# Optimization experiments

Measured on AMD Instinct MI355X. Metric: run time of the kernel, lower is better.

Reference implementation:

```python
import jax, jax.numpy as jnp
import numpy as np

DIM = 768
NUM_HEADS = 12
HEAD_DIM = DIM // NUM_HEADS
PATCH_H = 64
PATCH_W = 64
SCALE = HEAD_DIM ** -0.5


def setup_inputs() -> dict:
    key = jax.random.key(0)
    k1, k2, k3, k4 = jax.random.split(key, 4)
    x = jax.random.normal(k1, (16, PATCH_H * PATCH_W, DIM), dtype=jnp.float32)
    # torch Linear stores weight as (out, in); y = x @ W.T. Keep same convention.
    w_qkv = jax.random.normal(k2, (3 * DIM, DIM), dtype=jnp.float32) * (DIM ** -0.5)
    w_proj = jax.random.normal(k3, (DIM, DIM), dtype=jnp.float32) * (DIM ** -0.5)
    b_proj = jax.random.normal(k4, (DIM,), dtype=jnp.float32) * 0.01
    return {"x": x, "w_qkv": w_qkv, "w_proj": w_proj, "b_proj": b_proj}


def reference(x, w_qkv, w_proj, b_proj):
    B, N, C = x.shape
    H, W = PATCH_H, PATCH_W
    nh, hd = NUM_HEADS, HEAD_DIM
    # group rows: each row of W tokens attends only within itself
    xg = x.reshape(B * H, W, C)                      # (G, W, C)
    qkv = xg @ w_qkv.T                                # (G, W, 3C)
    qkv = qkv.reshape(B * H, W, 3, nh, hd)
    q = qkv[:, :, 0].transpose(0, 2, 1, 3)           # (G, nh, W, hd)
    k = qkv[:, :, 1].transpose(0, 2, 1, 3)
    v = qkv[:, :, 2].transpose(0, 2, 1, 3)
    attn = jnp.einsum('ghqd,ghkd->ghqk', q, k) * SCALE
    attn = jax.nn.softmax(attn, axis=-1)
    out = jnp.einsum('ghqk,ghkd->ghqd', attn, v)      # (G, nh, W, hd)
    out = out.transpose(0, 2, 1, 3).reshape(B * H, W, C)
    out = out @ w_proj.T + b_proj
    return out.reshape(B, N, C)
```

## Files before the change

### kernel.cpp

```cpp
#include <hip/hip_runtime.h>


#define SCALE 0.125f

typedef _Float16 h16;
typedef h16   half8 __attribute__((ext_vector_type(8)));
typedef float f32x4 __attribute__((ext_vector_type(4)));

typedef const __attribute__((address_space(1))) unsigned int ga_u32;
typedef __attribute__((address_space(3))) unsigned int ls_u32;

__device__ __forceinline__ void cvt8(const float* __restrict__ s,
                                     h16* __restrict__ d, int i) {
  const float4 a = ((const float4*)s)[2 * i];
  const float4 b = ((const float4*)s)[2 * i + 1];
  half8 r;
  r[0] = (h16)a.x; r[1] = (h16)a.y; r[2] = (h16)a.z; r[3] = (h16)a.w;
  r[4] = (h16)b.x; r[5] = (h16)b.y; r[6] = (h16)b.z; r[7] = (h16)b.w;
  ((half8*)d)[i] = r;
}

__global__ void prep_cvt(const float* __restrict__ wq, const float* __restrict__ wp,
                         const float* __restrict__ x,
                         h16* __restrict__ wq16, h16* __restrict__ wp16,
                         h16* __restrict__ xh) {
  const int stride = gridDim.x * blockDim.x;
  const int t0 = blockIdx.x * blockDim.x + threadIdx.x;
  for (int i = t0; i < 221184; i += stride) cvt8(wq, wq16, i);
  for (int i = t0; i < 73728;  i += stride) cvt8(wp, wp16, i);
  for (int i = t0; i < 6291456; i += stride) cvt8(x, xh, i);
}

__global__ void prep_w_only(const float* __restrict__ wq, const float* __restrict__ wp,
                            h16* __restrict__ wq16, h16* __restrict__ wp16) {
  const int stride = gridDim.x * blockDim.x;
  const int t0 = blockIdx.x * blockDim.x + threadIdx.x;
  for (int i = t0; i < 221184; i += stride) cvt8(wq, wq16, i);
  for (int i = t0; i < 73728;  i += stride) cvt8(wp, wp16, i);
}

__global__ __launch_bounds__(256)
void qkv_attn(const h16* __restrict__ A,
              const h16* __restrict__ B,
              h16* __restrict__ O) {
  __shared__ h16 smem[40960];
  h16* As0 = smem;
  h16* Bs0 = smem + 16384;
  h16* sQ  = smem;
  h16* sK  = smem + 9216;
  h16* sV  = smem + 18432;

  const int nwg = gridDim.x;
  const int bid = blockIdx.x;
  const int wg  = (bid & 7) * (nwg >> 3) + (bid >> 3);
  const int mt = wg / 12, h = wg - mt * 12;
  const int m0 = mt * 128;

  const int tid  = threadIdx.x;
  const int lane = tid & 63;
  const int wv   = tid >> 6;
  const int l16  = lane & 15;
  const int kg   = lane >> 4;
  const int wr   = wv >> 1;
  const int wc   = wv & 1;

  const int srow = tid >> 3;
  const int cg   = (tid & 7) ^ (srow & 7);
  const h16* pA[4];
  const h16* pB[6];
  int loA[4], loB[6];
  #pragma unroll
  for (int i = 0; i < 4; ++i) {
    const int r = i * 32 + srow;
    pA[i]  = A + (size_t)(m0 + r) * 768 + cg * 8;
    loA[i] = (i * 256 + tid) * 8;
  }
  #pragma unroll
  for (int i = 0; i < 6; ++i) {
    const int r  = i * 32 + srow;
    const int gr = (r >> 6) * 768 + h * 64 + (r & 63);
    pB[i]  = B + (size_t)gr * 768 + cg * 8;
    loB[i] = (i * 256 + tid) * 8;
  }

#define GLDS(srcp, ldsp)                                                       \
  __builtin_amdgcn_global_load_lds((ga_u32*)(const void*)(srcp),               \
                                   (ls_u32*)(void*)(ldsp), 16, 0, 0)
#define STAGE(bf, kt)                                                          \
  do {                                                                         \
    GLDS(pA[0] + (kt) * 64, &As0[(bf) * 8192 + loA[0]]);                       \
    GLDS(pA[1] + (kt) * 64, &As0[(bf) * 8192 + loA[1]]);                       \
    GLDS(pA[2] + (kt) * 64, &As0[(bf) * 8192 + loA[2]]);                       \
    GLDS(pA[3] + (kt) * 64, &As0[(bf) * 8192 + loA[3]]);                       \
    GLDS(pB[0] + (kt) * 64, &Bs0[(bf) * 12288 + loB[0]]);                      \
    GLDS(pB[1] + (kt) * 64, &Bs0[(bf) * 12288 + loB[1]]);                      \
    GLDS(pB[2] + (kt) * 64, &Bs0[(bf) * 12288 + loB[2]]);                      \
    GLDS(pB[3] + (kt) * 64, &Bs0[(bf) * 12288 + loB[3]]);                      \
    GLDS(pB[4] + (kt) * 64, &Bs0[(bf) * 12288 + loB[4]]);                      \
    GLDS(pB[5] + (kt) * 64, &Bs0[(bf) * 12288 + loB[5]]);                      \
  } while (0)

  const int aBase = (wr * 64 + l16) * 64;
  const int bBase = (wc * 96 + l16) * 64;
  int axor[2];
  #pragma unroll
  for (int ks = 0; ks < 2; ++ks)
    axor[ks] = ((ks * 4 + kg) ^ (l16 & 7)) * 8;

  f32x4 acc[4][6];
  #pragma unroll
  for (int mi = 0; mi < 4; ++mi)
    #pragma unroll
    for (int ni = 0; ni < 6; ++ni)
      acc[mi][ni] = (f32x4){0.f, 0.f, 0.f, 0.f};

  STAGE(0, 0);
  asm volatile("s_waitcnt vmcnt(0)" ::: "memory");
  __syncthreads();

  int cur = 0;
  for (int t = 0; t < 12; ++t) {
    if (t < 11) STAGE(cur ^ 1, t + 1);
    const h16* Ac = As0 + cur * 8192;
    const h16* Bc = Bs0 + cur * 12288;
    #pragma unroll
    for (int ks = 0; ks < 2; ++ks) {
      half8 af[4], bf8[6];
      #pragma unroll
      for (int mi = 0; mi < 4; ++mi)
        af[mi] = *(const half8*)&Ac[aBase + mi * 1024 + axor[ks]];
      #pragma unroll
      for (int ni = 0; ni < 6; ++ni)
        bf8[ni] = *(const half8*)&Bc[bBase + ni * 1024 + axor[ks]];
      #pragma unroll
      for (int mi = 0; mi < 4; ++mi)
        #pragma unroll
        for (int ni = 0; ni < 6; ++ni)
          acc[mi][ni] = __builtin_amdgcn_mfma_f32_16x16x32_f16(af[mi], bf8[ni], acc[mi][ni], 0, 0, 0);
    }
    asm volatile("s_waitcnt vmcnt(0)" ::: "memory");
    __syncthreads();
    cur ^= 1;
  }
#undef STAGE
#undef GLDS

  #pragma unroll
  for (int mi = 0; mi < 4; ++mi) {
    const int rowb = wr * 64 + mi * 16 + kg * 4;
    const int r6   = (rowb & 63);
    #pragma unroll
    for (int ni = 0; ni < 6; ++ni) {
      const int cbase = wc * 96 + ni * 16;
      const int sel = cbase >> 6;
      const int d   = (cbase & 63) + l16;
      if (sel == 0) {
        #pragma unroll
        for (int j = 0; j < 4; ++j) sQ[(rowb + j) * 72 + d] = (h16)acc[mi][ni][j];
      } else if (sel == 1) {
        #pragma unroll
        for (int j = 0; j < 4; ++j) sK[(rowb + j) * 72 + d] = (h16)acc[mi][ni][j];
      } else {
        #pragma unroll
        for (int j = 0; j < 4; ++j) sV[wr * 4608 + d * 72 + r6 + j] = (h16)acc[mi][ni][j];
      }
    }
  }
  __syncthreads();

  const int qr0 = wr * 64 + wc * 32;

  f32x4 sacc[2][4];
  #pragma unroll
  for (int rb = 0; rb < 2; ++rb)
    #pragma unroll
    for (int cb = 0; cb < 4; ++cb) sacc[rb][cb] = (f32x4){0.f, 0.f, 0.f, 0.f};

  #pragma unroll
  for (int ks = 0; ks < 2; ++ks) {
    half8 aq[2];
    #pragma unroll
    for (int rb = 0; rb < 2; ++rb)
      aq[rb] = *(const half8*)&sQ[(qr0 + rb * 16 + l16) * 72 + ks * 32 + kg * 8];
    #pragma unroll
    for (int cb = 0; cb < 4; ++cb) {
      const half8 kf = *(const half8*)&sK[(wr * 64 + cb * 16 + l16) * 72 + ks * 32 + kg * 8];
      #pragma unroll
      for (int rb = 0; rb < 2; ++rb)
        sacc[rb][cb] = __builtin_amdgcn_mfma_f32_16x16x32_f16(aq[rb], kf, sacc[rb][cb], 0, 0, 0);
    }
  }

  float e[2][4][4];
  #pragma unroll
  for (int rb = 0; rb < 2; ++rb) {
    float rs[4];
    #pragma unroll
    for (int j = 0; j < 4; ++j) {
      float t = 0.f;
      #pragma unroll
      for (int cb = 0; cb < 4; ++cb) { e[rb][cb][j] = __expf(sacc[rb][cb][j] * SCALE); t += e[rb][cb][j]; }
      rs[j] = t;
    }
    #pragma unroll
    for (int m = 1; m < 16; m <<= 1)
      #pragma unroll
      for (int j = 0; j < 4; ++j) rs[j] += __shfl_xor(rs[j], m);
    #pragma unroll
    for (int j = 0; j < 4; ++j) rs[j] = __fdividef(1.0f, rs[j]);
    #pragma unroll
    for (int cb = 0; cb < 4; ++cb)
      #pragma unroll
      for (int j = 0; j < 4; ++j)
        sQ[(qr0 + rb * 16 + kg * 4 + j) * 72 + cb * 16 + l16] = (h16)(e[rb][cb][j] * rs[j]);
  }
  __syncthreads();

  f32x4 oacc[2][4];
  #pragma unroll
  for (int rb = 0; rb < 2; ++rb)
    #pragma unroll
    for (int cb = 0; cb < 4; ++cb) oacc[rb][cb] = (f32x4){0.f, 0.f, 0.f, 0.f};
  #pragma unroll
  for (int ks = 0; ks < 2; ++ks) {
    half8 ap[2];
    #pragma unroll
    for (int rb = 0; rb < 2; ++rb)
      ap[rb] = *(const half8*)&sQ[(qr0 + rb * 16 + l16) * 72 + ks * 32 + kg * 8];
    #pragma unroll
    for (int cb = 0; cb < 4; ++cb) {
      const half8 vf = *(const half8*)&sV[wr * 4608 + (cb * 16 + l16) * 72 + ks * 32 + kg * 8];
      #pragma unroll
      for (int rb = 0; rb < 2; ++rb)
        oacc[rb][cb] = __builtin_amdgcn_mfma_f32_16x16x32_f16(ap[rb], vf, oacc[rb][cb], 0, 0, 0);
    }
  }

  #pragma unroll
  for (int rb = 0; rb < 2; ++rb)
    #pragma unroll
    for (int cb = 0; cb < 4; ++cb)
      #pragma unroll
      for (int j = 0; j < 4; ++j)
        sK[(qr0 + rb * 16 + kg * 4 + j) * 72 + cb * 16 + l16] = (h16)oacc[rb][cb][j];
  __syncthreads();
  #pragma unroll
  for (int c = tid; c < 1024; c += 256) {
    const int row = c >> 3, d0 = (c & 7) * 8;
    *(half8*)(O + (size_t)(m0 + row) * 768 + h * 64 + d0) = *(const half8*)&sK[row * 72 + d0];
  }
}

template <bool BIAS, typename OutT>
__global__ void gemm_bt(const h16* __restrict__ A, int lda,
                        const h16* __restrict__ B,
                        const float* __restrict__ bias,
                        OutT* __restrict__ C, int ldc,
                        int ntiles) {
  __shared__ h16 As[2][4096];
  __shared__ h16 Bs[2][4096];

  const int nwg = gridDim.x;
  const int bid = blockIdx.x;
  const int wg  = (bid & 7) * (nwg >> 3) + (bid >> 3);
  const int mt = wg / ntiles, nt = wg - mt * ntiles;
  const int m0 = mt * 128, n0 = nt * 128;

  const int tid  = threadIdx.x;
  const int lane = tid & 63;
  const int wv   = tid >> 6;
  const int l16  = lane & 15;
  const int kg   = lane >> 4;

  const h16* pa[2];
  const h16* pb[2];
  int lo[2];
  #pragma unroll
  for (int i = 0; i < 2; ++i) {
    const int row = wv * 32 + i * 16 + (lane >> 2);
    const int cg  = (lane & 3) ^ ((row >> 1) & 3);
    pa[i] = A + (size_t)(m0 + row) * lda + cg * 8;
    pb[i] = B + (size_t)(n0 + row) * 768 + cg * 8;
    lo[i] = wv * 1024 + i * 512;
  }

#define STAGE(bf, koff)                                                        \
  do {                                                                         \
    __builtin_amdgcn_global_load_lds((ga_u32*)(const void*)(pa[0] + (koff)),   \
                                     (ls_u32*)(void*)&As[bf][lo[0]], 16, 0, 0);\
    __builtin_amdgcn_global_load_lds((ga_u32*)(const void*)(pb[0] + (koff)),   \
                                     (ls_u32*)(void*)&Bs[bf][lo[0]], 16, 0, 0);\
    __builtin_amdgcn_global_load_lds((ga_u32*)(const void*)(pa[1] + (koff)),   \
                                     (ls_u32*)(void*)&As[bf][lo[1]], 16, 0, 0);\
    __builtin_amdgcn_global_load_lds((ga_u32*)(const void*)(pb[1] + (koff)),   \
                                     (ls_u32*)(void*)&Bs[bf][lo[1]], 16, 0, 0);\
  } while (0)

  const int s   = (l16 >> 1) & 3;
  const int wr  = wv >> 1, wc = wv & 1;
  const int ofA = (wr * 64 + l16) * 32 + ((kg ^ s) * 8);
  const int ofB = (wc * 64 + l16) * 32 + ((kg ^ s) * 8);

  f32x4 acc[4][4];
  #pragma unroll
  for (int mi = 0; mi < 4; ++mi)
    #pragma unroll
    for (int ni = 0; ni < 4; ++ni)
      acc[mi][ni] = (f32x4){0.f, 0.f, 0.f, 0.f};

  STAGE(0, 0);
  asm volatile("s_waitcnt vmcnt(0)" ::: "memory");
  __syncthreads();

  int cur = 0;
  for (int t = 0; t < 24; ++t) {
    if (t < 23) STAGE(cur ^ 1, (t + 1) * 32);
    half8 af[4], bf8[4];
    #pragma unroll
    for (int mi = 0; mi < 4; ++mi) af[mi]  = *(const half8*)&As[cur][ofA + mi * 512];
    #pragma unroll
    for (int ni = 0; ni < 4; ++ni) bf8[ni] = *(const half8*)&Bs[cur][ofB + ni * 512];
    #pragma unroll
    for (int mi = 0; mi < 4; ++mi)
      #pragma unroll
      for (int ni = 0; ni < 4; ++ni)
        acc[mi][ni] = __builtin_amdgcn_mfma_f32_16x16x32_f16(af[mi], bf8[ni], acc[mi][ni], 0, 0, 0);
    asm volatile("s_waitcnt vmcnt(0)" ::: "memory");
    __syncthreads();
    cur ^= 1;
  }
#undef STAGE

  float bv[4];
  if (BIAS) {
    #pragma unroll
    for (int ni = 0; ni < 4; ++ni) bv[ni] = bias[n0 + wc * 64 + ni * 16 + l16];
  }
  #pragma unroll
  for (int mi = 0; mi < 4; ++mi) {
    #pragma unroll
    for (int ni = 0; ni < 4; ++ni) {
      const int col = n0 + wc * 64 + ni * 16 + l16;
      #pragma unroll
      for (int j = 0; j < 4; ++j) {
        const int row = m0 + wr * 64 + mi * 16 + kg * 4 + j;
        if (BIAS) C[(size_t)row * ldc + col] = (OutT)(acc[mi][ni][j] + bv[ni]);
        else      C[(size_t)row * ldc + col] = (OutT)acc[mi][ni][j];
      }
    }
  }
}

template <typename WT>
__device__ __forceinline__ half8 loadw8(const WT* p);
template <>
__device__ __forceinline__ half8 loadw8<h16>(const h16* p) { return *(const half8*)p; }
template <>
__device__ __forceinline__ half8 loadw8<float>(const float* p) {
  const float4 a = *(const float4*)p;
  const float4 b = *(const float4*)(p + 4);
  half8 r;
  r[0] = (h16)a.x; r[1] = (h16)a.y; r[2] = (h16)a.z; r[3] = (h16)a.w;
  r[4] = (h16)b.x; r[5] = (h16)b.y; r[6] = (h16)b.z; r[7] = (h16)b.w;
  return r;
}

template <typename WT>
__launch_bounds__(512, 2)
__global__ void fused_fb(const float* __restrict__ x,
                         const WT* __restrict__ wq,
                         const WT* __restrict__ wp,
                         const float* __restrict__ bias,
                         float* __restrict__ out) {
  __shared__ h16   xs[64][776];
  __shared__ h16   qs[64][72];
  __shared__ h16   ks[64][72];
  __shared__ h16   vt[64][72];
  __shared__ float sS[64][68];

  const int g = blockIdx.x, tid = threadIdx.x;
  const int wv = tid >> 6, lane = tid & 63, l16 = lane & 15, kg = lane >> 4;

  const float* xg = x + (size_t)g * (64 * 768);
  #pragma unroll
  for (int i = 0; i < 24; ++i) {
    const int idx = tid + i * 512;
    const int row = idx / 192;
    const int c4  = (idx - row * 192) * 4;
    const float4 v = ((const float4*)xg)[idx];
    h16* p = &xs[row][c4];
    p[0] = (h16)v.x; p[1] = (h16)v.y; p[2] = (h16)v.z; p[3] = (h16)v.w;
  }

  f32x4 acc[4][6];
  #pragma unroll
  for (int a = 0; a < 4; ++a)
    #pragma unroll
    for (int b = 0; b < 6; ++b) acc[a][b] = (f32x4){0.f, 0.f, 0.f, 0.f};

  float bcol[6];
  #pragma unroll
  for (int cb = 0; cb < 6; ++cb) bcol[cb] = bias[wv * 96 + cb * 16 + l16];

  const int r0 = (wv & 1) * 32, c0 = (wv >> 1) * 48;
  const int rS = (wv >> 1) * 16, cS = (wv & 1) * 32;
  __syncthreads();

  for (int h = 0; h < 12; ++h) {
    f32x4 facc[2][3];
    #pragma unroll
    for (int a = 0; a < 2; ++a)
      #pragma unroll
      for (int b = 0; b < 3; ++b) facc[a][b] = (f32x4){0.f, 0.f, 0.f, 0.f};
    int wrow[3];
    #pragma unroll
    for (int cb = 0; cb < 3; ++cb) {
      const int n = c0 + cb * 16;
      wrow[cb] = (n >> 6) * 768 + h * 64 + (n & 63) + l16;
    }
    for (int k0 = 0; k0 < 768; k0 += 32) {
      const half8 a0 = *(const half8*)&xs[r0 + l16][k0 + kg * 8];
      const half8 a1 = *(const half8*)&xs[r0 + 16 + l16][k0 + kg * 8];
      #pragma unroll
      for (int cb = 0; cb < 3; ++cb) {
        const half8 b = loadw8<WT>(wq + (size_t)wrow[cb] * 768 + k0 + kg * 8);
        facc[0][cb] = __builtin_amdgcn_mfma_f32_16x16x32_f16(a0, b, facc[0][cb], 0, 0, 0);
        facc[1][cb] = __builtin_amdgcn_mfma_f32_16x16x32_f16(a1, b, facc[1][cb], 0, 0, 0);
      }
    }
    #pragma unroll
    for (int rb = 0; rb < 2; ++rb)
      #pragma unroll
      for (int cb = 0; cb < 3; ++cb) {
        const int col = c0 + cb * 16 + l16;
        const int rowb = r0 + rb * 16 + kg * 4;
        if (col < 64) {
          #pragma unroll
          for (int j = 0; j < 4; ++j) qs[rowb + j][col] = (h16)facc[rb][cb][j];
        } else if (col < 128) {
          #pragma unroll
          for (int j = 0; j < 4; ++j) ks[rowb + j][col - 64] = (h16)facc[rb][cb][j];
        } else {
          #pragma unroll
          for (int j = 0; j < 4; ++j) vt[col - 128][rowb + j] = (h16)facc[rb][cb][j];
        }
      }
    __syncthreads();

    f32x4 sacc[2];
    sacc[0] = (f32x4){0.f, 0.f, 0.f, 0.f};
    sacc[1] = (f32x4){0.f, 0.f, 0.f, 0.f};
    #pragma unroll
    for (int k0 = 0; k0 < 64; k0 += 32) {
      const half8 aq = *(const half8*)&qs[rS + l16][k0 + kg * 8];
      const half8 b0 = *(const half8*)&ks[cS + l16][k0 + kg * 8];
      const half8 b1 = *(const half8*)&ks[cS + 16 + l16][k0 + kg * 8];
      sacc[0] = __builtin_amdgcn_mfma_f32_16x16x32_f16(aq, b0, sacc[0], 0, 0, 0);
      sacc[1] = __builtin_amdgcn_mfma_f32_16x16x32_f16(aq, b1, sacc[1], 0, 0, 0);
    }
    #pragma unroll
    for (int t = 0; t < 2; ++t)
      #pragma unroll
      for (int j = 0; j < 4; ++j)
        sS[rS + kg * 4 + j][cS + t * 16 + l16] = sacc[t][j] * SCALE;
    __syncthreads();

    {
      const int row = tid >> 3, j0 = (tid & 7) * 8;
      float v0[8];
      #pragma unroll
      for (int i = 0; i < 8; ++i) v0[i] = sS[row][j0 + i];
      float m = v0[0];
      #pragma unroll
      for (int i = 1; i < 8; ++i) m = fmaxf(m, v0[i]);
      m = fmaxf(m, __shfl_xor(m, 1));
      m = fmaxf(m, __shfl_xor(m, 2));
      m = fmaxf(m, __shfl_xor(m, 4));
      float e[8], ssum = 0.f;
      #pragma unroll
      for (int i = 0; i < 8; ++i) { e[i] = __expf(v0[i] - m); ssum += e[i]; }
      ssum += __shfl_xor(ssum, 1);
      ssum += __shfl_xor(ssum, 2);
      ssum += __shfl_xor(ssum, 4);
      const float inv = 1.0f / ssum;
      #pragma unroll
      for (int i = 0; i < 8; ++i) qs[row][j0 + i] = (h16)(e[i] * inv);
    }
    __syncthreads();

    f32x4 oacc[2];
    oacc[0] = (f32x4){0.f, 0.f, 0.f, 0.f};
    oacc[1] = (f32x4){0.f, 0.f, 0.f, 0.f};
    #pragma unroll
    for (int k0 = 0; k0 < 64; k0 += 32) {
      const half8 ap = *(const half8*)&qs[rS + l16][k0 + kg * 8];
      const half8 b0 = *(const half8*)&vt[cS + l16][k0 + kg * 8];
      const half8 b1 = *(const half8*)&vt[cS + 16 + l16][k0 + kg * 8];
      oacc[0] = __builtin_amdgcn_mfma_f32_16x16x32_f16(ap, b0, oacc[0], 0, 0, 0);
      oacc[1] = __builtin_amdgcn_mfma_f32_16x16x32_f16(ap, b1, oacc[1], 0, 0, 0);
    }
    #pragma unroll
    for (int t = 0; t < 2; ++t)
      #pragma unroll
      for (int j = 0; j < 4; ++j)
        ks[rS + kg * 4 + j][cS + t * 16 + l16] = (h16)oacc[t][j];
    __syncthreads();

    #pragma unroll
    for (int k0 = 0; k0 < 64; k0 += 32) {
      half8 ah[4];
      #pragma unroll
      for (int rb = 0; rb < 4; ++rb)
        ah[rb] = *(const half8*)&ks[rb * 16 + l16][k0 + kg * 8];
      #pragma unroll
      for (int cb = 0; cb < 6; ++cb) {
        const int ocol = wv * 96 + cb * 16 + l16;
        const half8 bw = loadw8<WT>(wp + (size_t)ocol * 768 + h * 64 + k0 + kg * 8);
        #pragma unroll
        for (int rb = 0; rb < 4; ++rb)
          acc[rb][cb] = __builtin_amdgcn_mfma_f32_16x16x32_f16(ah[rb], bw, acc[rb][cb], 0, 0, 0);
      }
    }
    __syncthreads();
  }

  float* og = out + (size_t)g * (64 * 768);
  #pragma unroll
  for (int rb = 0; rb < 4; ++rb)
    #pragma unroll
    for (int cb = 0; cb < 6; ++cb) {
      const int col = wv * 96 + cb * 16 + l16;
      #pragma unroll
      for (int j = 0; j < 4; ++j) {
        const int row = rb * 16 + kg * 4 + j;
        og[(size_t)row * 768 + col] = acc[rb][cb][j] + bcol[cb];
      }
    }
}

extern "C" void kernel_launch(void* const* d_in, const int* in_sizes, int n_in,
                              void* d_out, int out_size, void* d_ws, size_t ws_size,
                              hipStream_t stream) {
  const float* x     = (const float*)d_in[0];
  const float* wqkv  = (const float*)d_in[1];
  const float* wproj = (const float*)d_in[2];
  const float* bias  = (const float*)d_in[3];
  float* out = (float*)d_out;

  const size_t SZ_WQ = (size_t)2304 * 768 * sizeof(h16);
  const size_t SZ_WP = (size_t)768 * 768 * sizeof(h16);
  const size_t SZ_XH = (size_t)65536 * 768 * sizeof(h16);
  const size_t SZ_O  = (size_t)65536 * 768 * sizeof(h16);

  if (ws_size >= SZ_WQ + SZ_WP + SZ_XH + SZ_O) {
    h16* wq16 = (h16*)d_ws;
    h16* wp16 = (h16*)((char*)d_ws + SZ_WQ);
    h16* xh   = (h16*)((char*)d_ws + SZ_WQ + SZ_WP);
    h16* obuf = (h16*)((char*)d_ws + SZ_WQ + SZ_WP + SZ_XH);

    prep_cvt<<<2048, 256, 0, stream>>>(wqkv, wproj, x, wq16, wp16, xh);
    qkv_attn<<<6144, 256, 0, stream>>>(xh, wq16, obuf);
    gemm_bt<true, float><<<3072, 256, 0, stream>>>(obuf, 768, wp16, bias, out, 768, 6);
  } else if (ws_size >= SZ_WQ + SZ_WP) {
    h16* wq16 = (h16*)d_ws;
    h16* wp16 = (h16*)((char*)d_ws + SZ_WQ);
    prep_w_only<<<512, 256, 0, stream>>>(wqkv, wproj, wq16, wp16);
    fused_fb<h16><<<1024, 512, 0, stream>>>(x, wq16, wp16, bias, out);
  } else {
    fused_fb<float><<<1024, 512, 0, stream>>>(x, wqkv, wproj, bias, out);
  }
}
```

Baseline: 476.3 us.

## Use 512-thread blocks in fused QKV-attention kernel with XOR-swizzled LDS layout

Doubles the qkv_attn workgroup from 4 to 8 waves, so each wave computes a 32x96 QKV tile instead of 64x96 and handles 16 query rows in attention instead of 32. This halves the accumulator registers per wave, which can raise occupancy and hide latency. The padded stride-72 LDS layout for Q/K/V is replaced by an XOR-swizzled stride-64 layout, with a matching unswizzle on the final store. The cost is more waves contending for the same LDS tiles and extra barrier participants. Per-wave B-fragment reuse also drops.

```diff
diff --git a/kernel.cpp b/kernel.cpp
--- a/kernel.cpp
+++ b/kernel.cpp
@@ -9,6 +9,8 @@
 
 typedef const __attribute__((address_space(1))) unsigned int ga_u32;
 typedef __attribute__((address_space(3))) unsigned int ls_u32;
+
+#define SWZ(r, c) (((r) << 6) + ((((c) >> 3) ^ ((r) & 7)) << 3) + ((c) & 7))
 
 __device__ __forceinline__ void cvt8(const float* __restrict__ s,
                                      h16* __restrict__ d, int i) {
@@ -39,7 +41,7 @@
   for (int i = t0; i < 73728;  i += stride) cvt8(wp, wp16, i);
 }
 
-__global__ __launch_bounds__(256)
+__global__ __launch_bounds__(512, 4)
 void qkv_attn(const h16* __restrict__ A,
               const h16* __restrict__ B,
               h16* __restrict__ O) {
@@ -47,8 +49,8 @@
   h16* As0 = smem;
   h16* Bs0 = smem + 16384;
   h16* sQ  = smem;
-  h16* sK  = smem + 9216;
-  h16* sV  = smem + 18432;
+  h16* sK  = smem + 8192;
+  h16* sV  = smem + 16384;
 
   const int nwg = gridDim.x;
   const int bid = blockIdx.x;
@@ -61,26 +63,27 @@
   const int wv   = tid >> 6;
   const int l16  = lane & 15;
   const int kg   = lane >> 4;
-  const int wr   = wv >> 1;
-  const int wc   = wv & 1;
+  const int wr   = wv & 3;
+  const int wc   = wv >> 2;
 
   const int srow = tid >> 3;
-  const int cg   = (tid & 7) ^ (srow & 7);
-  const h16* pA[4];
-  const h16* pB[6];
-  int loA[4], loB[6];
-  #pragma unroll
-  for (int i = 0; i < 4; ++i) {
-    const int r = i * 32 + srow;
+  const int slot = tid & 7;
+  const int cg   = slot ^ (srow & 7);
+  const h16* pA[2];
+  const h16* pB[3];
+  int loA[2], loB[3];
+  #pragma unroll
+  for (int i = 0; i < 2; ++i) {
+    const int r = i * 64 + srow;
     pA[i]  = A + (size_t)(m0 + r) * 768 + cg * 8;
-    loA[i] = (i * 256 + tid) * 8;
-  }
-  #pragma unroll
-  for (int i = 0; i < 6; ++i) {
-    const int r  = i * 32 + srow;
+    loA[i] = r * 64 + slot * 8;
+  }
+  #pragma unroll
+  for (int i = 0; i < 3; ++i) {
+    const int r  = i * 64 + srow;
     const int gr = (r >> 6) * 768 + h * 64 + (r & 63);
     pB[i]  = B + (size_t)gr * 768 + cg * 8;
-    loB[i] = (i * 256 + tid) * 8;
+    loB[i] = r * 64 + slot * 8;
   }
 
 #define GLDS(srcp, ldsp)                                                       \
@@ -90,26 +93,21 @@
   do {                                                                         \
     GLDS(pA[0] + (kt) * 64, &As0[(bf) * 8192 + loA[0]]);                       \
     GLDS(pA[1] + (kt) * 64, &As0[(bf) * 8192 + loA[1]]);                       \
-    GLDS(pA[2] + (kt) * 64, &As0[(bf) * 8192 + loA[2]]);                       \
-    GLDS(pA[3] + (kt) * 64, &As0[(bf) * 8192 + loA[3]]);                       \
     GLDS(pB[0] + (kt) * 64, &Bs0[(bf) * 12288 + loB[0]]);                      \
     GLDS(pB[1] + (kt) * 64, &Bs0[(bf) * 12288 + loB[1]]);                      \
     GLDS(pB[2] + (kt) * 64, &Bs0[(bf) * 12288 + loB[2]]);                      \
-    GLDS(pB[3] + (kt) * 64, &Bs0[(bf) * 12288 + loB[3]]);                      \
-    GLDS(pB[4] + (kt) * 64, &Bs0[(bf) * 12288 + loB[4]]);                      \
-    GLDS(pB[5] + (kt) * 64, &Bs0[(bf) * 12288 + loB[5]]);                      \
   } while (0)
 
-  const int aBase = (wr * 64 + l16) * 64;
+  const int aBase = (wr * 32 + l16) * 64;
   const int bBase = (wc * 96 + l16) * 64;
   int axor[2];
   #pragma unroll
   for (int ks = 0; ks < 2; ++ks)
     axor[ks] = ((ks * 4 + kg) ^ (l16 & 7)) * 8;
 
-  f32x4 acc[4][6];
-  #pragma unroll
-  for (int mi = 0; mi < 4; ++mi)
+  f32x4 acc[2][6];
+  #pragma unroll
+  for (int mi = 0; mi < 2; ++mi)
     #pragma unroll
     for (int ni = 0; ni < 6; ++ni)
       acc[mi][ni] = (f32x4){0.f, 0.f, 0.f, 0.f};
@@ -125,15 +123,15 @@
     const h16* Bc = Bs0 + cur * 12288;
     #pragma unroll
     for (int ks = 0; ks < 2; ++ks) {
-      half8 af[4], bf8[6];
-      #pragma unroll
-      for (int mi = 0; mi < 4; ++mi)
+      half8 af[2], bf8[6];
+      #pragma unroll
+      for (int mi = 0; mi < 2; ++mi)
         af[mi] = *(const half8*)&Ac[aBase + mi * 1024 + axor[ks]];
       #pragma unroll
       for (int ni = 0; ni < 6; ++ni)
         bf8[ni] = *(const half8*)&Bc[bBase + ni * 1024 + axor[ks]];
       #pragma unroll
-      for (int mi = 0; mi < 4; ++mi)
+      for (int mi = 0; mi < 2; ++mi)
         #pragma unroll
         for (int ni = 0; ni < 6; ++ni)
           acc[mi][ni] = __builtin_amdgcn_mfma_f32_16x16x32_f16(af[mi], bf8[ni], acc[mi][ni], 0, 0, 0);
@@ -146,9 +144,10 @@
 #undef GLDS
 
   #pragma unroll
-  for (int mi = 0; mi < 4; ++mi) {
-    const int rowb = wr * 64 + mi * 16 + kg * 4;
-    const int r6   = (rowb & 63);
+  for (int mi = 0; mi < 2; ++mi) {
+    const int rowb = wr * 32 + mi * 16 + kg * 4;
+    const int r6   = rowb & 63;
+    const int g2s  = rowb >> 6;
     #pragma unroll
     for (int ni = 0; ni < 6; ++ni) {
       const int cbase = wc * 96 + ni * 16;
@@ -156,98 +155,83 @@
       const int d   = (cbase & 63) + l16;
       if (sel == 0) {
         #pragma unroll
-        for (int j = 0; j < 4; ++j) sQ[(rowb + j) * 72 + d] = (h16)acc[mi][ni][j];
+        for (int j = 0; j < 4; ++j) sQ[SWZ(rowb + j, d)] = (h16)acc[mi][ni][j];
       } else if (sel == 1) {
         #pragma unroll
-        for (int j = 0; j < 4; ++j) sK[(rowb + j) * 72 + d] = (h16)acc[mi][ni][j];
+        for (int j = 0; j < 4; ++j) sK[SWZ(rowb + j, d)] = (h16)acc[mi][ni][j];
       } else {
         #pragma unroll
-        for (int j = 0; j < 4; ++j) sV[wr * 4608 + d * 72 + r6 + j] = (h16)acc[mi][ni][j];
+        for (int j = 0; j < 4; ++j) sV[g2s * 4096 + SWZ(d, r6 + j)] = (h16)acc[mi][ni][j];
       }
     }
   }
   __syncthreads();
 
-  const int qr0 = wr * 64 + wc * 32;
-
-  f32x4 sacc[2][4];
-  #pragma unroll
-  for (int rb = 0; rb < 2; ++rb)
-    #pragma unroll
-    for (int cb = 0; cb < 4; ++cb) sacc[rb][cb] = (f32x4){0.f, 0.f, 0.f, 0.f};
-
+  const int qr0 = wv * 16;
+  const int g2  = wv >> 2;
+  const h16* sKg = sK + g2 * 4096;
+  const h16* sVg = sV + g2 * 4096;
+
+  f32x4 sacc[4];
+  #pragma unroll
+  for (int cb = 0; cb < 4; ++cb) sacc[cb] = (f32x4){0.f, 0.f, 0.f, 0.f};
   #pragma unroll
   for (int ks = 0; ks < 2; ++ks) {
-    half8 aq[2];
-    #pragma unroll
-    for (int rb = 0; rb < 2; ++rb)
-      aq[rb] = *(const half8*)&sQ[(qr0 + rb * 16 + l16) * 72 + ks * 32 + kg * 8];
+    const half8 aq = *(const half8*)&sQ[(qr0 + l16) * 64 + axor[ks]];
     #pragma unroll
     for (int cb = 0; cb < 4; ++cb) {
-      const half8 kf = *(const half8*)&sK[(wr * 64 + cb * 16 + l16) * 72 + ks * 32 + kg * 8];
-      #pragma unroll
-      for (int rb = 0; rb < 2; ++rb)
-        sacc[rb][cb] = __builtin_amdgcn_mfma_f32_16x16x32_f16(aq[rb], kf, sacc[rb][cb], 0, 0, 0);
-    }
-  }
-
-  float e[2][4][4];
-  #pragma unroll
-  for (int rb = 0; rb < 2; ++rb) {
-    float rs[4];
-    #pragma unroll
-    for (int j = 0; j < 4; ++j) {
-      float t = 0.f;
-      #pragma unroll
-      for (int cb = 0; cb < 4; ++cb) { e[rb][cb][j] = __expf(sacc[rb][cb][j] * SCALE); t += e[rb][cb][j]; }
-      rs[j] = t;
-    }
-    #pragma unroll
-    for (int m = 1; m < 16; m <<= 1)
-      #pragma unroll
-      for (int j = 0; j < 4; ++j) rs[j] += __shfl_xor(rs[j], m);
-    #pragma unroll
-    for (int j = 0; j < 4; ++j) rs[j] = __fdividef(1.0f, rs[j]);
-    #pragma unroll
-    for (int cb = 0; cb < 4; ++cb)
-      #pragma unroll
-      for (int j = 0; j < 4; ++j)
-        sQ[(qr0 + rb * 16 + kg * 4 + j) * 72 + cb * 16 + l16] = (h16)(e[rb][cb][j] * rs[j]);
-  }
+      const half8 kf = *(const half8*)&sKg[(cb * 16 + l16) * 64 + axor[ks]];
+      sacc[cb] = __builtin_amdgcn_mfma_f32_16x16x32_f16(aq, kf, sacc[cb], 0, 0, 0);
+    }
+  }
+
+  float e[4][4], rs[4];
+  #pragma unroll
+  for (int j = 0; j < 4; ++j) {
+    float t = 0.f;
+    #pragma unroll
+    for (int cb = 0; cb < 4; ++cb) { e[cb][j] = __expf(sacc[cb][j] * SCALE); t += e[cb][j]; }
+    rs[j] = t;
+  }
+  #pragma unroll
+  for (int m = 1; m < 16; m <<= 1)
+    #pragma unroll
+    for (int j = 0; j < 4; ++j) rs[j] += __shfl_xor(rs[j], m);
+  #pragma unroll
+  for (int j = 0; j < 4; ++j) rs[j] = __fdividef(1.0f, rs[j]);
+
+  #pragma unroll
+  for (int cb = 0; cb < 4; ++cb)
+    #pragma unroll
+    for (int j = 0; j < 4; ++j)
+      sQ[SWZ(qr0 + kg * 4 + j, cb * 16 + l16)] = (h16)(e[cb][j] * rs[j]);
   __syncthreads();
 
-  f32x4 oacc[2][4];
-  #pragma unroll
-  for (int rb = 0; rb < 2; ++rb)
-    #pragma unroll
-    for (int cb = 0; cb < 4; ++cb) oacc[rb][cb] = (f32x4){0.f, 0.f, 0.f, 0.f};
+  f32x4 oacc[4];
+  #pragma unroll
+  for (int cb = 0; cb < 4; ++cb) oacc[cb] = (f32x4){0.f, 0.f, 0.f, 0.f};
   #pragma unroll
   for (int ks = 0; ks < 2; ++ks) {
-    half8 ap[2];
-    #pragma unroll
-    for (int rb = 0; rb < 2; ++rb)
-      ap[rb] = *(const half8*)&sQ[(qr0 + rb * 16 + l16) * 72 + ks * 32 + kg * 8];
+    const half8 ap = *(const half8*)&sQ[(qr0 + l16) * 64 + axor[ks]];
     #pragma unroll
     for (int cb = 0; cb < 4; ++cb) {
-      const half8 vf = *(const half8*)&sV[wr * 4608 + (cb * 16 + l16) * 72 + ks * 32 + kg * 8];
-      #pragma unroll
-      for (int rb = 0; rb < 2; ++rb)
-        oacc[rb][cb] = __builtin_amdgcn_mfma_f32_16x16x32_f16(ap[rb], vf, oacc[rb][cb], 0, 0, 0);
-    }
-  }
-
-  #pragma unroll
-  for (int rb = 0; rb < 2; ++rb)
-    #pragma unroll
-    for (int cb = 0; cb < 4; ++cb)
-      #pragma unroll
-      for (int j = 0; j < 4; ++j)
-        sK[(qr0 + rb * 16 + kg * 4 + j) * 72 + cb * 16 + l16] = (h16)oacc[rb][cb][j];
+      const half8 vf = *(const half8*)&sVg[(cb * 16 + l16) * 64 + axor[ks]];
+      oacc[cb] = __builtin_amdgcn_mfma_f32_16x16x32_f16(ap, vf, oacc[cb], 0, 0, 0);
+    }
+  }
+
+  #pragma unroll
+  for (int cb = 0; cb < 4; ++cb)
+    #pragma unroll
+    for (int j = 0; j < 4; ++j)
+      sK[SWZ(qr0 + kg * 4 + j, cb * 16 + l16)] = (h16)oacc[cb][j];
   __syncthreads();
   #pragma unroll
-  for (int c = tid; c < 1024; c += 256) {
-    const int row = c >> 3, d0 = (c & 7) * 8;
-    *(half8*)(O + (size_t)(m0 + row) * 768 + h * 64 + d0) = *(const half8*)&sK[row * 72 + d0];
+  for (int c = tid; c < 1024; c += 512) {
+    const int row = c >> 3, sl = c & 7;
+    const int gch = sl ^ (row & 7);
+    *(half8*)(O + (size_t)(m0 + row) * 768 + h * 64 + gch * 8) =
+        *(const half8*)&sK[row * 64 + sl * 8];
   }
 }
 
@@ -559,7 +543,7 @@
     h16* obuf = (h16*)((char*)d_ws + SZ_WQ + SZ_WP + SZ_XH);
 
     prep_cvt<<<2048, 256, 0, stream>>>(wqkv, wproj, x, wq16, wp16, xh);
-    qkv_attn<<<6144, 256, 0, stream>>>(xh, wq16, obuf);
+    qkv_attn<<<6144, 512, 0, stream>>>(xh, wq16, obuf);
     gemm_bt<true, float><<<3072, 256, 0, stream>>>(obuf, 768, wp16, bias, out, 768, 6);
   } else if (ws_size >= SZ_WQ + SZ_WP) {
     h16* wq16 = (h16*)d_ws;
```

Result: faster. 444.8 us (-6.6%).
